# Optimization experiments

Measured on AMD Instinct MI355X. Metric: run time of the kernel, lower is better.

## Reference

```python
import jax, jax.numpy as jnp
import numpy as np

B, S, E, H = 4, 8192, 512, 8
D = E // H  # head_dim = 64


def setup_inputs() -> dict:
    key = jax.random.key(0)
    ks = jax.random.split(key, 9)
    scale = 1.0 / np.sqrt(E)
    x = jax.random.normal(ks[0], (B, S, E), dtype=jnp.float32)
    # torch nn.Linear convention: y = x @ W.T + b, W has shape (out, in)
    Wp = jax.random.uniform(ks[1], (E, E), jnp.float32, -scale, scale)
    bp = jax.random.uniform(ks[2], (E,), jnp.float32, -scale, scale)
    Wc = jax.random.uniform(ks[3], (E, E), jnp.float32, -scale, scale)
    bc = jax.random.uniform(ks[4], (E,), jnp.float32, -scale, scale)
    Ws = jax.random.uniform(ks[5], (E, E), jnp.float32, -scale, scale)
    bs = jax.random.uniform(ks[6], (E,), jnp.float32, -scale, scale)
    Wo = jax.random.uniform(ks[7], (E, E), jnp.float32, -scale, scale)
    bo = jax.random.uniform(ks[8], (E,), jnp.float32, -scale, scale)
    return {"x": x, "Wp": Wp, "bp": bp, "Wc": Wc, "bc": bc,
            "Ws": Ws, "bs": bs, "Wo": Wo, "bo": bo}


def reference(x, Wp, bp, Wc, bc, Ws, bs, Wo, bo):
    # Faithful to TreeAttention.forward with tree_structure=None (default path).
    # NOTE: original views projections as (B,S,H,D) without transposing head/seq,
    # so the matmuls mix HEADS per token (HxH scores), not tokens.
    b, s, _ = x.shape
    parent = (jnp.einsum('bse,fe->bsf', x, Wp) + bp).reshape(b, s, H, D)
    child = (jnp.einsum('bse,fe->bsf', x, Wc) + bc).reshape(b, s, H, D)
    sibling = (jnp.einsum('bse,fe->bsf', x, Ws) + bs).reshape(b, s, H, D)
    # per-token head-mixing scores: (B, S, H, H)
    scores = jnp.einsum('bshd,bstd->bsht', parent, child) / jnp.sqrt(
        jnp.asarray(D, dtype=x.dtype))
    attention = jax.nn.softmax(scores, axis=-1)
    # dropout is identity in eval mode (reference runs in inference mode)
    out = jnp.einsum('bsht,bstd->bshd', attention, sibling).reshape(b, s, E)
    return jnp.einsum('bse,fe->bsf', out, Wo) + bo
```

## Files before the change

### kernel.cpp

```cpp
#include <hip/hip_runtime.h>
#include <hip/hip_bf16.h>

typedef unsigned short u16;
typedef __attribute__((ext_vector_type(8))) short bf16x8;
typedef __attribute__((ext_vector_type(4))) float f32x4;
typedef __attribute__((ext_vector_type(8))) unsigned short u16x8;

#define GLDS(gp, lp) __builtin_amdgcn_global_load_lds( \
    (const __attribute__((address_space(1))) void*)(gp), \
    (__attribute__((address_space(3))) void*)(lp), 16, 0, 0)

__device__ __forceinline__ u16 f2b(float f) {
  unsigned u = __builtin_bit_cast(unsigned, f);
  return (u16)((u + 0x7fffu + ((u >> 16) & 1u)) >> 16);
}
__device__ __forceinline__ float b2f(u16 s) {
  return __builtin_bit_cast(float, (unsigned)s << 16);
}

#define BARX() do { __builtin_amdgcn_sched_barrier(0); \
  asm volatile("s_barrier" ::: "memory"); \
  __builtin_amdgcn_sched_barrier(0); } while (0)

__global__ __launch_bounds__(256) void convert_k(
    const float* __restrict__ x, const float* __restrict__ Wp,
    const float* __restrict__ Wc, const float* __restrict__ Ws,
    const float* __restrict__ Wo, u16* __restrict__ xb,
    u16* __restrict__ wall, u16* __restrict__ wob)
{
  const long CX = 2097152;
  const long CW = 98304;
  const long CO = 32768;
  const long total = CX + CW + CO;
  for (long i = (long)blockIdx.x * blockDim.x + threadIdx.x; i < total;
       i += (long)gridDim.x * blockDim.x) {
    const float* src; u16* dst;
    if (i < CX) {
      src = x + i * 8; dst = xb + i * 8;
    } else if (i < CX + CW) {
      long e = (i - CX) * 8;
      int n = (int)(e >> 9), k = (int)(e & 511);
      const float* wr = (n < 512)  ? (Wp + (long)n * 512)
                      : (n < 1024) ? (Wc + (long)(n - 512) * 512)
                                   : (Ws + (long)(n - 1024) * 512);
      src = wr + k; dst = wall + e;
    } else {
      long e = (i - CX - CW) * 8; src = Wo + e; dst = wob + e;
    }
    f32x4 v0 = *(const f32x4*)src;
    f32x4 v1 = *(const f32x4*)(src + 4);
    u16x8 o;
    o[0]=f2b(v0[0]); o[1]=f2b(v0[1]); o[2]=f2b(v0[2]); o[3]=f2b(v0[3]);
    o[4]=f2b(v1[0]); o[5]=f2b(v1[1]); o[6]=f2b(v1[2]); o[7]=f2b(v1[3]);
    *(u16x8*)dst = o;
  }
}

template<int NC, bool BF16OUT>
__global__ __launch_bounds__(512, 2) void gemm8(
    const u16* __restrict__ A, const u16* __restrict__ Bw,
    const float* __restrict__ bias0, const float* __restrict__ bias1,
    const float* __restrict__ bias2, void* __restrict__ Cout)
{
  __shared__ alignas(16) char smem[65536];
  char* sAc = smem;
  char* sBc = smem + 32768;

  const int tid = threadIdx.x;
  const int w = tid >> 6, lane = tid & 63;
  const int wr = w >> 2, wc = w & 3;
  const int ln15 = lane & 15, g4 = lane >> 4, l7 = lane & 7;

  const int nbx = NC / 256;
  const int nwg = nbx * 128;
  const int qq = nwg / 8;
  const int flat = blockIdx.x;
  const int swz = (flat & 7) * qq + (flat >> 3);
  const int bx = swz % nbx, by = swz / nbx;
  const long row0 = (long)by * 256;
  const int col0 = bx * 256;

  const int t8 = tid >> 3;
  const int gsw = (tid & 7) ^ (t8 & 7);
  const u16* pA = A + (row0 + t8) * 512 + gsw * 8;
  const u16* pB = Bw + ((long)col0 + (t8 >> 5) * 64 + (t8 & 31)) * 512 + gsw * 8;

#define STG_A(h, t) do { \
    const u16* s_ = pA + (h) * 32768 + (t) * 64; \
    char* d_ = sAc + (h) * 16384 + w * 1024; \
    GLDS(s_, d_); GLDS(s_ + 65536, d_ + 8192); \
  } while (0)
#define STG_B(h, t) do { \
    const u16* s_ = pB + (h) * 16384 + (t) * 64; \
    char* d_ = sBc + (h) * 16384 + w * 1024; \
    GLDS(s_, d_); GLDS(s_ + 65536, d_ + 8192); \
  } while (0)

  const int gkb0 = (g4 ^ l7) << 4;
  const int gkb1 = ((g4 + 4) ^ l7) << 4;
  const int aoff = (wr * 64 + ln15) * 128;
  const int boff = (wc * 32 + ln15) * 128;

#define LOAD_A(MH) do { \
    const char* ba_ = sAc + (MH) * 16384 + aoff; \
    _Pragma("unroll") for (int mf = 0; mf < 4; ++mf) { \
      aF[mf][0] = *(const bf16x8*)(ba_ + mf * 2048 + gkb0); \
      aF[mf][1] = *(const bf16x8*)(ba_ + mf * 2048 + gkb1); \
    } } while (0)
#define LOAD_B(NH, BF) do { \
    const char* bb_ = sBc + (NH) * 16384 + boff; \
    _Pragma("unroll") for (int nf = 0; nf < 2; ++nf) { \
      BF[nf][0] = *(const bf16x8*)(bb_ + nf * 2048 + gkb0); \
      BF[nf][1] = *(const bf16x8*)(bb_ + nf * 2048 + gkb1); \
    } } while (0)
#define MFMA_Q(MH, NH, BF) do { \
    __builtin_amdgcn_s_setprio(1); \
    _Pragma("unroll") for (int mf = 0; mf < 4; ++mf) \
    _Pragma("unroll") for (int nf = 0; nf < 2; ++nf) { \
      f32x4 c_ = acc[(MH) * 4 + mf][(NH) * 2 + nf]; \
      c_ = __builtin_amdgcn_mfma_f32_16x16x32_bf16(aF[mf][0], BF[nf][0], c_, 0, 0, 0); \
      c_ = __builtin_amdgcn_mfma_f32_16x16x32_bf16(aF[mf][1], BF[nf][1], c_, 0, 0, 0); \
      acc[(MH) * 4 + mf][(NH) * 2 + nf] = c_; \
    } \
    __builtin_amdgcn_s_setprio(0); \
  } while (0)
#define VMW(nstr) asm volatile("s_waitcnt vmcnt(" nstr ")" ::: "memory")

  f32x4 acc[8][4] = {};

  STG_A(0, 0); STG_B(0, 0); STG_B(1, 0); STG_A(1, 0);

  for (int t = 0; t < 8; ++t) {
    const bool st = (t < 7);
    bf16x8 aF[4][2], bFa[2][2], bFb[2][2];

    VMW("4"); BARX();
    LOAD_A(0); LOAD_B(0, bFa);
    MFMA_Q(0, 0, bFa);
    VMW("2"); BARX();
    if (st) { STG_A(0, t + 1); STG_B(0, t + 1); }
    LOAD_B(1, bFb);
    MFMA_Q(0, 1, bFb);
    if (st) VMW("4"); else VMW("0");
    BARX();
    if (st) STG_B(1, t + 1);
    LOAD_A(1);
    MFMA_Q(1, 1, bFb);
    BARX();
    if (st) STG_A(1, t + 1);
    MFMA_Q(1, 0, bFa);
  }

  __syncthreads();
  const long rgb = row0 + wr * 128;
  const int cgb = col0 + wc * 64;
  if (BF16OUT) {
    u16* sc = (u16*)(smem + (w << 13));
#pragma unroll
    for (int h2 = 0; h2 < 2; ++h2) {
#pragma unroll
      for (int n = 0; n < 4; ++n) {
        const int colg = cgb + ln15 + n * 16;
        const float* bp_ = (NC == 512) ? bias0
                           : (colg < 512 ? bias0 : (colg < 1024 ? bias1 : bias2));
        const float bv = bp_[colg & 511];
        const int c = ln15 + n * 16;
        const int gsl = c >> 3, co = c & 7;
#pragma unroll
        for (int mf = 0; mf < 4; ++mf)
#pragma unroll
          for (int j = 0; j < 4; ++j) {
            const int r = mf * 16 + (g4 << 2) + j;
            sc[r * 64 + (((gsl ^ (r & 7)) << 3) | co)] = f2b(acc[h2 * 4 + mf][n][j] + bv);
          }
      }
      asm volatile("s_waitcnt lgkmcnt(0)" ::: "memory");
      __builtin_amdgcn_sched_barrier(0);
#pragma unroll
      for (int it = 0; it < 8; ++it) {
        const int rr = it * 8 + (lane >> 3);
        const int gl = lane & 7;
        u16x8 v = *(const u16x8*)(sc + rr * 64 + ((gl ^ (rr & 7)) << 3));
        *(u16x8*)((u16*)Cout + (rgb + h2 * 64 + rr) * NC + cgb + gl * 8) = v;
      }
      asm volatile("s_waitcnt lgkmcnt(0)" ::: "memory");
      __builtin_amdgcn_sched_barrier(0);
    }
  } else {
    float* scf = (float*)(smem + (w << 13));
#pragma unroll
    for (int q = 0; q < 4; ++q) {
#pragma unroll
      for (int n = 0; n < 4; ++n) {
        const int colg = cgb + ln15 + n * 16;
        const float bv = bias0[colg & 511];
        const int c = ln15 + n * 16;
        const int gsl = c >> 2, co = c & 3;
#pragma unroll
        for (int mh = 0; mh < 2; ++mh)
#pragma unroll
          for (int j = 0; j < 4; ++j) {
            const int r = mh * 16 + (g4 << 2) + j;
            scf[r * 64 + (((gsl ^ (r & 7)) << 2) | co)] = acc[q * 2 + mh][n][j] + bv;
          }
      }
      asm volatile("s_waitcnt lgkmcnt(0)" ::: "memory");
      __builtin_amdgcn_sched_barrier(0);
#pragma unroll
      for (int it = 0; it < 8; ++it) {
        const int rr = it * 4 + (lane >> 4);
        const int gl = lane & 15;
        f32x4 v = *(const f32x4*)(scf + rr * 64 + ((gl ^ (rr & 7)) << 2));
        *(f32x4*)((float*)Cout + (rgb + q * 32 + rr) * NC + cgb + gl * 4) = v;
      }
      asm volatile("s_waitcnt lgkmcnt(0)" ::: "memory");
      __builtin_amdgcn_sched_barrier(0);
    }
  }
#undef STG_A
#undef STG_B
#undef LOAD_A
#undef LOAD_B
#undef MFMA_Q
#undef VMW
}

__global__ __launch_bounds__(256) void attn_k(const u16* __restrict__ PCS,
                                              u16* __restrict__ OUT)
{
  __shared__ float L[4][1664];
  const int w = threadIdx.x >> 6, lane = threadIdx.x & 63;
  const long token = (long)blockIdx.x * 4 + w;
  float* Lw = L[w];
  const int C0 = 544, S0 = 1088, AT0 = 1600;
  const u16* rowp = PCS + token * 1536;
#pragma unroll
  for (int q = 0; q < 3; ++q) {
    u16x8 v = *(const u16x8*)(rowp + q * 512 + lane * 8);
    float* dst = (q < 2) ? (Lw + q * 544 + (lane >> 3) * 68 + (lane & 7) * 8)
                         : (Lw + S0 + lane * 8);
    f32x4 a = {b2f(v[0]), b2f(v[1]), b2f(v[2]), b2f(v[3])};
    f32x4 b = {b2f(v[4]), b2f(v[5]), b2f(v[6]), b2f(v[7])};
    *(f32x4*)dst = a;
    *(f32x4*)(dst + 4) = b;
  }
  const int h = lane >> 3, t = lane & 7;
  float sc = 0.f;
#pragma unroll
  for (int d = 0; d < 64; d += 4) {
    f32x4 pv = *(const f32x4*)(Lw + h * 68 + d);
    f32x4 cv = *(const f32x4*)(Lw + C0 + t * 68 + d);
    sc += pv[0]*cv[0] + pv[1]*cv[1] + pv[2]*cv[2] + pv[3]*cv[3];
  }
  sc *= 0.125f;
  float mx = sc;
  mx = fmaxf(mx, __shfl_xor(mx, 1));
  mx = fmaxf(mx, __shfl_xor(mx, 2));
  mx = fmaxf(mx, __shfl_xor(mx, 4));
  float e = __expf(sc - mx);
  float sm = e;
  sm += __shfl_xor(sm, 1);
  sm += __shfl_xor(sm, 2);
  sm += __shfl_xor(sm, 4);
  Lw[AT0 + lane] = e / sm;
  float o[8] = {0, 0, 0, 0, 0, 0, 0, 0};
#pragma unroll
  for (int tt = 0; tt < 8; ++tt) {
    const float av = Lw[AT0 + h * 8 + tt];
    f32x4 s0 = *(const f32x4*)(Lw + S0 + tt * 64 + t * 8);
    f32x4 s1 = *(const f32x4*)(Lw + S0 + tt * 64 + t * 8 + 4);
    o[0] += av * s0[0]; o[1] += av * s0[1]; o[2] += av * s0[2]; o[3] += av * s0[3];
    o[4] += av * s1[0]; o[5] += av * s1[1]; o[6] += av * s1[2]; o[7] += av * s1[3];
  }
  u16x8 ov;
#pragma unroll
  for (int j = 0; j < 8; ++j) ov[j] = f2b(o[j]);
  *(u16x8*)(OUT + token * 512 + lane * 8) = ov;
}

extern "C" void kernel_launch(void* const* d_in, const int* in_sizes, int n_in,
                              void* d_out, int out_size, void* d_ws, size_t ws_size,
                              hipStream_t stream) {
  const float* x  = (const float*)d_in[0];
  const float* Wp = (const float*)d_in[1];
  const float* bp = (const float*)d_in[2];
  const float* Wc = (const float*)d_in[3];
  const float* bc = (const float*)d_in[4];
  const float* Ws = (const float*)d_in[5];
  const float* bs = (const float*)d_in[6];
  const float* Wo = (const float*)d_in[7];
  const float* bo = (const float*)d_in[8];

  char* ws = (char*)d_ws;
  u16* xb   = (u16*)ws;
  u16* wall = (u16*)(ws + 33554432);
  u16* wob  = (u16*)(ws + 35127296);
  u16* pcs  = (u16*)(ws + 35651584);
  u16* outb = xb;

  convert_k<<<2048, 256, 0, stream>>>(x, Wp, Wc, Ws, Wo, xb, wall, wob);
  gemm8<1536, true><<<768, 512, 0, stream>>>(xb, wall, bp, bc, bs, pcs);
  attn_k<<<8192, 256, 0, stream>>>(pcs, outb);
  gemm8<512, false><<<256, 512, 0, stream>>>(outb, wob, bo, bo, bo, d_out);
}
```

Measured before the change: 133.2 us.

## Pre-swizzle weights into MFMA fragment order and load B directly to registers

The convert kernel now writes the packed QKV weights and Wo in a 16-row-tiled layout that matches the MFMA B-fragment order. The GEMM then reads B fragments straight from global memory into registers, skipping LDS staging for B and halving LDS traffic and barriers per k-step. The cost is that B loads are issued just before use and are duplicated across the two wave rows. This can expose global/L2 latency inside the MFMA loop, and the vmcnt bookkeeping changes.

```diff
diff --git a/kernel.cpp b/kernel.cpp
--- a/kernel.cpp
+++ b/kernel.cpp
@@ -43,9 +43,13 @@
       const float* wr = (n < 512)  ? (Wp + (long)n * 512)
                       : (n < 1024) ? (Wc + (long)(n - 512) * 512)
                                    : (Ws + (long)(n - 1024) * 512);
-      src = wr + k; dst = wall + e;
+      src = wr + k;
+      dst = wall + (long)(n >> 4) * 8192 + (k >> 3) * 128 + (n & 15) * 8;
     } else {
-      long e = (i - CX - CW) * 8; src = Wo + e; dst = wob + e;
+      long e = (i - CX - CW) * 8;
+      int n = (int)(e >> 9), k = (int)(e & 511);
+      src = Wo + e;
+      dst = wob + (long)(n >> 4) * 8192 + (k >> 3) * 128 + (n & 15) * 8;
     }
     f32x4 v0 = *(const f32x4*)src;
     f32x4 v1 = *(const f32x4*)(src + 4);
@@ -64,7 +68,6 @@
 {
   __shared__ alignas(16) char smem[65536];
   char* sAc = smem;
-  char* sBc = smem + 32768;
 
   const int tid = threadIdx.x;
   const int w = tid >> 6, lane = tid & 63;
@@ -83,23 +86,16 @@
   const int t8 = tid >> 3;
   const int gsw = (tid & 7) ^ (t8 & 7);
   const u16* pA = A + (row0 + t8) * 512 + gsw * 8;
-  const u16* pB = Bw + ((long)col0 + (t8 >> 5) * 64 + (t8 & 31)) * 512 + gsw * 8;
 
 #define STG_A(h, t) do { \
     const u16* s_ = pA + (h) * 32768 + (t) * 64; \
     char* d_ = sAc + (h) * 16384 + w * 1024; \
     GLDS(s_, d_); GLDS(s_ + 65536, d_ + 8192); \
   } while (0)
-#define STG_B(h, t) do { \
-    const u16* s_ = pB + (h) * 16384 + (t) * 64; \
-    char* d_ = sBc + (h) * 16384 + w * 1024; \
-    GLDS(s_, d_); GLDS(s_ + 65536, d_ + 8192); \
-  } while (0)
 
   const int gkb0 = (g4 ^ l7) << 4;
   const int gkb1 = ((g4 + 4) ^ l7) << 4;
   const int aoff = (wr * 64 + ln15) * 128;
-  const int boff = (wc * 32 + ln15) * 128;
 
 #define LOAD_A(MH) do { \
     const char* ba_ = sAc + (MH) * 16384 + aoff; \
@@ -107,12 +103,15 @@
       aF[mf][0] = *(const bf16x8*)(ba_ + mf * 2048 + gkb0); \
       aF[mf][1] = *(const bf16x8*)(ba_ + mf * 2048 + gkb1); \
     } } while (0)
-#define LOAD_B(NH, BF) do { \
-    const char* bb_ = sBc + (NH) * 16384 + boff; \
-    _Pragma("unroll") for (int nf = 0; nf < 2; ++nf) { \
-      BF[nf][0] = *(const bf16x8*)(bb_ + nf * 2048 + gkb0); \
-      BF[nf][1] = *(const bf16x8*)(bb_ + nf * 2048 + gkb1); \
-    } } while (0)
+
+  const u16* pBg = Bw + ((long)(col0 >> 4) + wc * 4) * 8192 + g4 * 128 + ln15 * 8;
+
+#define GLB_B(NH, BF, t) do { \
+    _Pragma("unroll") for (int nf = 0; nf < 2; ++nf) \
+    _Pragma("unroll") for (int kk = 0; kk < 2; ++kk) \
+      BF[nf][kk] = *(const bf16x8*)(pBg + ((NH) * 2 + nf) * 8192 + ((t) * 8 + kk * 4) * 128); \
+  } while (0)
+
 #define MFMA_Q(MH, NH, BF) do { \
     __builtin_amdgcn_s_setprio(1); \
     _Pragma("unroll") for (int mf = 0; mf < 4; ++mf) \
@@ -128,22 +127,20 @@
 
   f32x4 acc[8][4] = {};
 
-  STG_A(0, 0); STG_B(0, 0); STG_B(1, 0); STG_A(1, 0);
+  STG_A(0, 0); STG_A(1, 0);
 
   for (int t = 0; t < 8; ++t) {
     const bool st = (t < 7);
     bf16x8 aF[4][2], bFa[2][2], bFb[2][2];
 
-    VMW("4"); BARX();
-    LOAD_A(0); LOAD_B(0, bFa);
+    VMW("2"); BARX();
+    GLB_B(0, bFa, t); GLB_B(1, bFb, t);
+    LOAD_A(0);
     MFMA_Q(0, 0, bFa);
+    BARX();
+    if (st) STG_A(0, t + 1);
+    MFMA_Q(0, 1, bFb);
     VMW("2"); BARX();
-    if (st) { STG_A(0, t + 1); STG_B(0, t + 1); }
-    LOAD_B(1, bFb);
-    MFMA_Q(0, 1, bFb);
-    if (st) VMW("4"); else VMW("0");
-    BARX();
-    if (st) STG_B(1, t + 1);
     LOAD_A(1);
     MFMA_Q(1, 1, bFb);
     BARX();
@@ -218,9 +215,8 @@
     }
   }
 #undef STG_A
-#undef STG_B
 #undef LOAD_A
-#undef LOAD_B
+#undef GLB_B
 #undef MFMA_Q
 #undef VMW
 }
```

Result: no change. 135.1 us (+1.4%).

## Triple-buffer A tiles in LDS to prefetch two k-steps ahead

Applied to the files above, without the earlier changes.

Grows the GEMM's shared memory from 64KB to 128KB so the A operand uses a 3-stage ring buffer, and A tiles are now issued two iterations ahead while B stays one ahead. The wait counts and barriers are reworked to match the deeper prefetch. The aim is to hide more global-load latency behind the MFMA work. The cost is that the larger LDS footprint cuts occupancy from the two workgroups per CU that the launch bounds request, and the hand-tuned vmcnt values are fragile.

```diff
diff --git a/kernel.cpp b/kernel.cpp
--- a/kernel.cpp
+++ b/kernel.cpp
@@ -62,9 +62,9 @@
     const float* __restrict__ bias0, const float* __restrict__ bias1,
     const float* __restrict__ bias2, void* __restrict__ Cout)
 {
-  __shared__ alignas(16) char smem[65536];
+  __shared__ alignas(16) char smem[131072];
   char* sAc = smem;
-  char* sBc = smem + 32768;
+  char* sBc = smem + 98304;
 
   const int tid = threadIdx.x;
   const int w = tid >> 6, lane = tid & 63;
@@ -85,13 +85,13 @@
   const u16* pA = A + (row0 + t8) * 512 + gsw * 8;
   const u16* pB = Bw + ((long)col0 + (t8 >> 5) * 64 + (t8 & 31)) * 512 + gsw * 8;
 
-#define STG_A(h, t) do { \
-    const u16* s_ = pA + (h) * 32768 + (t) * 64; \
-    char* d_ = sAc + (h) * 16384 + w * 1024; \
+#define STG_A(h, tt) do { \
+    const u16* s_ = pA + (h) * 32768 + (tt) * 64; \
+    char* d_ = sAc + ((tt) % 3) * 32768 + (h) * 16384 + w * 1024; \
     GLDS(s_, d_); GLDS(s_ + 65536, d_ + 8192); \
   } while (0)
-#define STG_B(h, t) do { \
-    const u16* s_ = pB + (h) * 16384 + (t) * 64; \
+#define STG_B(h, tt) do { \
+    const u16* s_ = pB + (h) * 16384 + (tt) * 64; \
     char* d_ = sBc + (h) * 16384 + w * 1024; \
     GLDS(s_, d_); GLDS(s_ + 65536, d_ + 8192); \
   } while (0)
@@ -102,7 +102,7 @@
   const int boff = (wc * 32 + ln15) * 128;
 
 #define LOAD_A(MH) do { \
-    const char* ba_ = sAc + (MH) * 16384 + aoff; \
+    const char* ba_ = bufA + (MH) * 16384 + aoff; \
     _Pragma("unroll") for (int mf = 0; mf < 4; ++mf) { \
       aF[mf][0] = *(const bf16x8*)(ba_ + mf * 2048 + gkb0); \
       aF[mf][1] = *(const bf16x8*)(ba_ + mf * 2048 + gkb1); \
@@ -128,26 +128,30 @@
 
   f32x4 acc[8][4] = {};
 
-  STG_A(0, 0); STG_B(0, 0); STG_B(1, 0); STG_A(1, 0);
+  STG_A(0, 0); STG_A(1, 0); STG_B(0, 0); STG_A(0, 1); STG_B(1, 0); STG_A(1, 1);
 
   for (int t = 0; t < 8; ++t) {
-    const bool st = (t < 7);
+    const bool stB = (t < 7);
+    const bool stA = (t < 6);
+    const char* bufA = sAc + (t % 3) * 32768;
     bf16x8 aF[4][2], bFa[2][2], bFb[2][2];
 
-    VMW("4"); BARX();
+    if (t < 7) { VMW("6"); } else { VMW("2"); }
+    BARX();
     LOAD_A(0); LOAD_B(0, bFa);
     MFMA_Q(0, 0, bFa);
-    VMW("2"); BARX();
-    if (st) { STG_A(0, t + 1); STG_B(0, t + 1); }
+    if (t < 7) { VMW("2"); } else { VMW("0"); }
+    BARX();
+    if (stB) STG_B(0, t + 1);
+    if (stA) STG_A(0, t + 2);
     LOAD_B(1, bFb);
     MFMA_Q(0, 1, bFb);
-    if (st) VMW("4"); else VMW("0");
     BARX();
-    if (st) STG_B(1, t + 1);
+    if (stB) STG_B(1, t + 1);
     LOAD_A(1);
     MFMA_Q(1, 1, bFb);
     BARX();
-    if (st) STG_A(1, t + 1);
+    if (stA) STG_A(1, t + 2);
     MFMA_Q(1, 0, bFa);
   }
 
```

Measured after the change: 132.4 us. Within noise of the previous version (-0.6%).
